# Optimization experiments

Hardware: AMD Instinct MI355X
Metric: run time of the kernel (lower is better)

Reference implementation:

```python
import jax, jax.numpy as jnp
import numpy as np

N, C, A, CI = 32768, 512, 64, 1024  # n_locations, content_size, address_size, controller_input_size
EPS = 1e-7


def setup_inputs() -> dict:
    key = jax.random.key(0)
    ks = jax.random.split(key, 12)
    g = lambda i, shape, s=1.0: jax.random.normal(ks[i], shape, dtype=jnp.float32) * s
    xav = lambda i, shape: g(i, shape, float(np.sqrt(2.0 / (shape[0] + shape[1]))))
    return {
        "controller_hidden_state": g(0, (N, 1)),
        "controller_input": g(1, (CI, 1)),
        "memory_contents": g(2, (N, C), 0.5),
        "memory_addresses": xav(3, (N, A)),
        "exp_mov_avg_similarity": g(4, (N, 1), 0.1),
        "W_query": xav(5, (C + A, N)),
        "b_query": jnp.zeros((C + A, 1), jnp.float32),
        "u_sharpen": xav(6, (1, N)),
        "b_sharpen": jnp.zeros((1,), jnp.float32),
        "u_lru": xav(7, (1, N)),
        "b_lru": jnp.zeros((1,), jnp.float32),
        "W_erase": xav(8, (C, N)),
        "b_erase": jnp.zeros((C, 1), jnp.float32),
        "W_content_hidden": xav(9, (C, N)),
        "W_content_input": xav(10, (C, CI)),
        "u_content_alpha": xav(11, (N + CI, 1)),
        "b_content_alpha": jnp.zeros((1, 1), jnp.float32),
    }


def reference(controller_hidden_state, controller_input, memory_contents, memory_addresses,
              exp_mov_avg_similarity, W_query, b_query, u_sharpen, b_sharpen, u_lru, b_lru,
              W_erase, b_erase, W_content_hidden, W_content_input, u_content_alpha,
              b_content_alpha):
    h, x = controller_hidden_state, controller_input
    # ---- address_memory ----
    full_mem = jnp.concatenate([memory_addresses, memory_contents], axis=1)  # [N, A+C]
    query = W_query @ h + b_query                                            # [A+C, 1]
    beta = jax.nn.softplus(u_sharpen @ h + b_sharpen) + 1.0                  # [1, 1]
    q = query[:, 0]
    q_norm = jnp.maximum(jnp.linalg.norm(q), EPS)
    m_norm = jnp.maximum(jnp.linalg.norm(full_mem, axis=1), EPS)             # [N]
    cos = (full_mem @ q) / (m_norm * q_norm)                                 # [N] cosine sim per location
    sim = (beta[0, 0] * cos)[:, None]                                        # [N, 1]
    gamma = jax.nn.sigmoid(u_lru @ h + b_lru)                                # [1, 1] LRU gate
    addr = jax.nn.softmax(sim - gamma * exp_mov_avg_similarity, axis=0)      # [N, 1]
    # (state buffer update, next-step only): new_ema = 0.1*ema + 0.9*sim
    # ---- update (vectorized erase/write over all N locations) ----
    erase = W_erase @ h + b_erase                                            # [C, 1]
    alpha = u_content_alpha.T @ jnp.concatenate([h, x], axis=0) + b_content_alpha  # [1, 1]
    cand = jax.nn.relu(W_content_hidden @ h + alpha * (W_content_input @ x))       # [C, 1]
    new_mem = (1.0 - addr * erase.T) * memory_contents + addr * cand.T       # [N, C]
    # ---- read (on updated memory) ----
    new_full = jnp.concatenate([memory_addresses, new_mem], axis=1)          # [N, A+C]
    read = new_full.T @ addr                                                 # [A+C, 1]
    return read
```

## Files before the change

### kernel.cpp

```cpp
#include <hip/hip_runtime.h>
#include <hip/hip_bf16.h>
#include <math.h>

#define NN 32768
#define CC 512
#define AA 64
#define CIN 1024
#define EPSV 1e-7f


#define QOFF 2128
#define STOFF 2704
#define SCOFF 4240
#define PAOFF 5264
#define PMOFF 38032

typedef float floatx4 __attribute__((ext_vector_type(4)));

__device__ __forceinline__ float4 ntload4(const float4* p) {
    floatx4 v = __builtin_nontemporal_load(reinterpret_cast<const floatx4*>(p));
    return make_float4(v.x, v.y, v.z, v.w);
}
__device__ __forceinline__ float ntloadf(const float* p) {
    return __builtin_nontemporal_load(p);
}

__global__ __launch_bounds__(256) void k1_gemv(
    const float* __restrict__ h, const float* __restrict__ x,
    const float* __restrict__ Wq, const float* __restrict__ Wer,
    const float* __restrict__ Wch, const float* __restrict__ Wci,
    const float* __restrict__ ush, const float* __restrict__ ulr,
    const float* __restrict__ uca, float* __restrict__ ws)
{
    const int b = blockIdx.x, tid = threadIdx.x;
    const int wave = tid >> 6, lane = tid & 63;
    __shared__ float hs[4096];
    __shared__ float red[4][8];

    if (b < 1600) {
        const int rg = b >> 3, chunk = b & 7;
        const float4* h4 = reinterpret_cast<const float4*>(h) + chunk * 1024;
        float4* hs4 = reinterpret_cast<float4*>(hs);
        #pragma unroll
        for (int k = 0; k < 4; ++k) hs4[k * 256 + tid] = h4[k * 256 + tid];
        __syncthreads();
        const int r0 = rg * 8;
        const float* mat; int base;
        if (r0 < 576)       { mat = Wq;  base = 0; }
        else if (r0 < 1088) { mat = Wer; base = 576; }
        else                { mat = Wch; base = 1088; }
        const float4* m4 = reinterpret_cast<const float4*>(
            mat + (size_t)(r0 - base) * NN + chunk * 4096);
        const int rs = NN / 4;
        float acc[8] = {0,0,0,0,0,0,0,0};
        float4 cur[8];
        #pragma unroll
        for (int r = 0; r < 8; ++r) cur[r] = ntload4(m4 + (size_t)r * rs + tid);
        #pragma unroll
        for (int it = 0; it < 4; ++it) {
            float4 nxt[8];
            if (it < 3) {
                #pragma unroll
                for (int r = 0; r < 8; ++r)
                    nxt[r] = ntload4(m4 + (size_t)r * rs + (it + 1) * 256 + tid);
            }
            float4 hb = hs4[it * 256 + tid];
            #pragma unroll
            for (int r = 0; r < 8; ++r)
                acc[r] += cur[r].x * hb.x + cur[r].y * hb.y +
                          cur[r].z * hb.z + cur[r].w * hb.w;
            if (it < 3) {
                #pragma unroll
                for (int r = 0; r < 8; ++r) cur[r] = nxt[r];
            }
        }
        #pragma unroll
        for (int r = 0; r < 8; ++r) {
            #pragma unroll
            for (int off = 32; off >= 1; off >>= 1)
                acc[r] += __shfl_xor(acc[r], off);
        }
        if (lane == 0) {
            #pragma unroll
            for (int r = 0; r < 8; ++r) red[wave][r] = acc[r];
        }
        __syncthreads();
        if (tid < 8) {
            float v = red[0][tid] + red[1][tid] + red[2][tid] + red[3][tid];
            atomicAdd(ws + r0 + tid, v);
        }
    } else if (b < 1664) {
        const int rg = b - 1600;
        float4 xv = reinterpret_cast<const float4*>(x)[tid];
        const float4* m4 = reinterpret_cast<const float4*>(
            Wci + (size_t)rg * 8 * CIN);
        float acc[8];
        #pragma unroll
        for (int r = 0; r < 8; ++r) {
            float4 a = ntload4(m4 + r * 256 + tid);
            acc[r] = a.x * xv.x + a.y * xv.y + a.z * xv.z + a.w * xv.w;
        }
        #pragma unroll
        for (int r = 0; r < 8; ++r) {
            #pragma unroll
            for (int off = 32; off >= 1; off >>= 1)
                acc[r] += __shfl_xor(acc[r], off);
        }
        if (lane == 0) {
            #pragma unroll
            for (int r = 0; r < 8; ++r) red[wave][r] = acc[r];
        }
        __syncthreads();
        if (tid < 8) {
            float v = red[0][tid] + red[1][tid] + red[2][tid] + red[3][tid];
            ws[1600 + rg * 8 + tid] = v;
        }
    } else {
        const int t = b - 1664, sd = t >> 3, chunk = t & 7;
        const float* vec = (sd == 0) ? ush : (sd == 1) ? ulr : uca;
        const float4* v4 = reinterpret_cast<const float4*>(vec) + chunk * 1024;
        const float4* h4 = reinterpret_cast<const float4*>(h) + chunk * 1024;
        float acc = 0.f;
        #pragma unroll
        for (int it = 0; it < 4; ++it) {
            float4 a = v4[it * 256 + tid];
            float4 hb = h4[it * 256 + tid];
            acc += a.x * hb.x + a.y * hb.y + a.z * hb.z + a.w * hb.w;
        }
        if (sd == 2 && chunk == 0) {
            float4 a = reinterpret_cast<const float4*>(uca)[NN / 4 + tid];
            float4 xv = reinterpret_cast<const float4*>(x)[tid];
            acc += a.x * xv.x + a.y * xv.y + a.z * xv.z + a.w * xv.w;
        }
        #pragma unroll
        for (int off = 32; off >= 1; off >>= 1)
            acc += __shfl_xor(acc, off);
        if (lane == 0) red[wave][0] = acc;
        __syncthreads();
        if (tid == 0)
            atomicAdd(ws + 2112 + sd,
                      red[0][0] + red[1][0] + red[2][0] + red[3][0]);
    }
}

__global__ __launch_bounds__(256) void k1b_scalars(
    const float* __restrict__ bq, const float* __restrict__ bsh,
    const float* __restrict__ blr, const float* __restrict__ bca,
    float* __restrict__ ws)
{
    __shared__ float red[256];
    const int tid = threadIdx.x;
    float s = 0.f;
    for (int j = tid; j < 576; j += 256) {
        float q = ws[j] + bq[j];
        ws[QOFF + j] = q;
        s += q * q;
    }
    red[tid] = s; __syncthreads();
    for (int st = 128; st > 0; st >>= 1) {
        if (tid < st) red[tid] += red[tid + st];
        __syncthreads();
    }
    if (tid == 0) {
        float qn = fmaxf(sqrtf(red[0]), EPSV);
        float bp = ws[2112] + bsh[0];
        float beta = (bp > 20.f ? bp : log1pf(expf(bp))) + 1.0f;
        float gp = ws[2113] + blr[0];
        float gamma = 1.f / (1.f + expf(-gp));
        float alpha = ws[2114] + bca[0];
        ws[2112] = beta; ws[2113] = gamma; ws[2114] = alpha; ws[2115] = qn;
    }
}

__global__ __launch_bounds__(512) void k2f_fused(
    const float* __restrict__ Mm, const float* __restrict__ Ad,
    const float* __restrict__ ema, const float* __restrict__ ws,
    float* __restrict__ pm, float* __restrict__ pa, float* __restrict__ stats)
{
    __shared__ float lw[8][1092];
    const int b = blockIdx.x, tid = threadIdx.x, wave = tid >> 6, lane = tid & 63;
    const float beta = ws[2112], gamma = ws[2113], qn = ws[2115];
    const float ql = ws[QOFF + lane];
    float4 qa = *reinterpret_cast<const float4*>(ws + QOFF + 64 + lane * 8);
    float4 qb = *reinterpret_cast<const float4*>(ws + QOFF + 68 + lane * 8);
    float qm[8] = {qa.x, qa.y, qa.z, qa.w, qb.x, qb.y, qb.z, qb.w};

    float a1[8] = {0,0,0,0,0,0,0,0};
    float a2[8] = {0,0,0,0,0,0,0,0};
    float aA = 0.f, m_run = -1e30f, Z = 0.f, S2 = 0.f;
    const int base = b * 64 + wave * 8;
    for (int j = 0; j < 8; ++j) {
        const int i = base + j;
        float a = ntloadf(Ad + (size_t)i * AA + lane);
        float4 m0 = ntload4(reinterpret_cast<const float4*>(Mm + (size_t)i * CC + lane * 8));
        float4 m1 = ntload4(reinterpret_cast<const float4*>(Mm + (size_t)i * CC + lane * 8 + 4));
        float mm[8] = {m0.x, m0.y, m0.z, m0.w, m1.x, m1.y, m1.z, m1.w};
        float dot = a * ql, nn = a * a;
        #pragma unroll
        for (int k = 0; k < 8; ++k) { float f = mm[k]; dot += f * qm[k]; nn += f * f; }
        #pragma unroll
        for (int off = 32; off >= 1; off >>= 1) {
            dot += __shfl_xor(dot, off);
            nn  += __shfl_xor(nn, off);
        }
        float mn = fmaxf(sqrtf(nn), EPSV);
        float s = beta * (dot / (mn * qn)) - gamma * ema[i];
        if (s > m_run) {
            float f = expf(m_run - s);
            float f2 = f * f;
            Z *= f; S2 *= f2; aA *= f;
            #pragma unroll
            for (int k = 0; k < 8; ++k) { a1[k] *= f; a2[k] *= f2; }
            m_run = s;
        }
        float w = expf(s - m_run);
        float w2 = w * w;
        Z += w; S2 += w2; aA += w * a;
        #pragma unroll
        for (int k = 0; k < 8; ++k) { a1[k] += w * mm[k]; a2[k] += w2 * mm[k]; }
    }
    #pragma unroll
    for (int k = 0; k < 8; ++k) {
        lw[wave][lane * 8 + k] = a1[k];
        lw[wave][512 + lane * 8 + k] = a2[k];
    }
    lw[wave][1024 + lane] = aA;
    if (lane == 0) { lw[wave][1088] = m_run; lw[wave][1089] = Z; lw[wave][1090] = S2; }
    __syncthreads();
    float mb = lw[0][1088];
    #pragma unroll
    for (int w = 1; w < 8; ++w) mb = fmaxf(mb, lw[w][1088]);
    float fw[8];
    #pragma unroll
    for (int w = 0; w < 8; ++w) fw[w] = expf(lw[w][1088] - mb);
    for (int e = tid; e < 1024; e += 512) {
        float v = 0.f;
        if (e < 512) {
            #pragma unroll
            for (int w = 0; w < 8; ++w) v += fw[w] * lw[w][e];
        } else {
            #pragma unroll
            for (int w = 0; w < 8; ++w) v += fw[w] * fw[w] * lw[w][e];
        }
        pm[(size_t)e * 512 + b] = v;
    }
    if (tid < 64) {
        float v = 0.f;
        #pragma unroll
        for (int w = 0; w < 8; ++w) v += fw[w] * lw[w][1024 + tid];
        pa[tid * 512 + b] = v;
    }
    if (tid == 0) {
        float Zl = 0.f, S2l = 0.f;
        #pragma unroll
        for (int w = 0; w < 8; ++w) {
            Zl  += fw[w] * lw[w][1089];
            S2l += fw[w] * fw[w] * lw[w][1090];
        }
        stats[b] = mb; stats[512 + b] = Zl; stats[1024 + b] = S2l;
    }
}

__global__ __launch_bounds__(512) void k3g(
    const float* __restrict__ stats, float* __restrict__ sc,
    float* __restrict__ ws)
{
    __shared__ float red[512];
    const int t = threadIdx.x;
    float m = stats[t];
    red[t] = m; __syncthreads();
    for (int st = 256; st > 0; st >>= 1) {
        if (t < st) red[t] = fmaxf(red[t], red[t + st]);
        __syncthreads();
    }
    float mx = red[0]; __syncthreads();
    float e1 = expf(m - mx);
    red[t] = e1 * stats[512 + t]; __syncthreads();
    for (int st = 256; st > 0; st >>= 1) {
        if (t < st) red[t] += red[t + st];
        __syncthreads();
    }
    float Zg = red[0]; __syncthreads();
    red[t] = e1 * e1 * stats[1024 + t]; __syncthreads();
    for (int st = 256; st > 0; st >>= 1) {
        if (t < st) red[t] += red[t + st];
        __syncthreads();
    }
    float S2s = red[0];
    float iZ = 1.f / Zg;
    sc[t] = e1 * iZ;
    sc[512 + t] = e1 * e1 * iZ * iZ;
    if (t == 0) ws[2118] = S2s * iZ * iZ;
}

__global__ __launch_bounds__(256) void k5_final(
    const float* __restrict__ ws, const float* __restrict__ pm,
    const float* __restrict__ pa, const float* __restrict__ sc,
    const float* __restrict__ ber, float* __restrict__ out)
{
    __shared__ float red[256];
    const int b = blockIdx.x, tid = threadIdx.x;
    if (b < 64) {
        float v = sc[tid] * pa[b * 512 + tid] + sc[tid + 256] * pa[b * 512 + tid + 256];
        red[tid] = v; __syncthreads();
        for (int st = 128; st > 0; st >>= 1) {
            if (tid < st) red[tid] += red[tid + st];
            __syncthreads();
        }
        if (tid == 0) out[b] = red[0];
    } else {
        const int c = b - 64;
        float v1 = sc[tid] * pm[(size_t)c * 512 + tid]
                 + sc[tid + 256] * pm[(size_t)c * 512 + tid + 256];
        float v2 = sc[512 + tid] * pm[(size_t)(512 + c) * 512 + tid]
                 + sc[512 + tid + 256] * pm[(size_t)(512 + c) * 512 + tid + 256];
        red[tid] = v1; __syncthreads();
        for (int st = 128; st > 0; st >>= 1) {
            if (tid < st) red[tid] += red[tid + st];
            __syncthreads();
        }
        float s1 = red[0];
        __syncthreads();
        red[tid] = v2; __syncthreads();
        for (int st = 128; st > 0; st >>= 1) {
            if (tid < st) red[tid] += red[tid + st];
            __syncthreads();
        }
        if (tid == 0) {
            float s2v = red[0];
            float er = ws[576 + c] + ber[c];
            float ch = ws[1088 + c], cx = ws[1600 + c];
            float alpha = ws[2114], S2 = ws[2118];
            float cand = fmaxf(ch + alpha * cx, 0.f);
            out[64 + c] = s1 - er * s2v + S2 * cand;
        }
    }
}

extern "C" void kernel_launch(void* const* d_in, const int* in_sizes, int n_in,
                              void* d_out, int out_size, void* d_ws, size_t ws_size,
                              hipStream_t stream)
{
    const float* h   = (const float*)d_in[0];
    const float* x   = (const float*)d_in[1];
    const float* Mm  = (const float*)d_in[2];
    const float* Ad  = (const float*)d_in[3];
    const float* ema = (const float*)d_in[4];
    const float* Wq  = (const float*)d_in[5];
    const float* bq  = (const float*)d_in[6];
    const float* ush = (const float*)d_in[7];
    const float* bsh = (const float*)d_in[8];
    const float* ulr = (const float*)d_in[9];
    const float* blr = (const float*)d_in[10];
    const float* Wer = (const float*)d_in[11];
    const float* ber = (const float*)d_in[12];
    const float* Wch = (const float*)d_in[13];
    const float* Wci = (const float*)d_in[14];
    const float* uca = (const float*)d_in[15];
    const float* bca = (const float*)d_in[16];

    float* ws    = (float*)d_ws;
    float* stats = ws + STOFF;
    float* sc    = ws + SCOFF;
    float* pa    = ws + PAOFF;
    float* pm    = ws + PMOFF;
    float* out   = (float*)d_out;

    (void)hipMemsetAsync(ws, 0, QOFF * sizeof(float), stream);

    hipLaunchKernelGGL(k1_gemv,     dim3(1688), dim3(256), 0, stream,
                       h, x, Wq, Wer, Wch, Wci, ush, ulr, uca, ws);
    hipLaunchKernelGGL(k1b_scalars, dim3(1),    dim3(256), 0, stream,
                       bq, bsh, blr, bca, ws);
    hipLaunchKernelGGL(k2f_fused,   dim3(512),  dim3(512), 0, stream,
                       Mm, Ad, ema, ws, pm, pa, stats);
    hipLaunchKernelGGL(k3g,         dim3(1),    dim3(512), 0, stream, stats, sc, ws);
    hipLaunchKernelGGL(k5_final,    dim3(576),  dim3(256), 0, stream,
                       ws, pm, pa, sc, ber, out);
}
```

Measured before the change: 281.3 us.

## Drop memset and two single-block kernels by writing per-chunk partials

The GEMV stage now writes per-chunk partial sums to distinct workspace slots instead of using atomicAdd. This removes the hipMemsetAsync that zeroed the accumulators. The scalar-prep kernel is folded into the prologue of the fused memory kernel, and the softmax-statistics kernel is recomputed redundantly in every block of the final kernel, leaving three launches instead of five plus a memset. Block reductions switch from shared-memory trees to wave shuffles. The cost is redundant per-block work: every block re-reduces the query partials, and 576 blocks each re-reduce the 512 softmax stats.

```diff
diff --git a/kernel.cpp b/kernel.cpp
--- a/kernel.cpp
+++ b/kernel.cpp
@@ -1,5 +1,4 @@
 #include <hip/hip_runtime.h>
-#include <hip/hip_bf16.h>
 #include <math.h>
 
 #define NN 32768
@@ -9,11 +8,12 @@
 #define EPSV 1e-7f
 
 
-#define QOFF 2128
-#define STOFF 2704
-#define SCOFF 4240
-#define PAOFF 5264
-#define PMOFF 38032
+#define DOTP  0
+#define SDOT  12800
+#define CONTX 12824
+#define STOFF 13344
+#define PAOFF 14912
+#define PMOFF 47680
 
 typedef float floatx4 __attribute__((ext_vector_type(4)));
 
@@ -87,7 +87,7 @@
         __syncthreads();
         if (tid < 8) {
             float v = red[0][tid] + red[1][tid] + red[2][tid] + red[3][tid];
-            atomicAdd(ws + r0 + tid, v);
+            ws[DOTP + chunk * 1600 + r0 + tid] = v;
         }
     } else if (b < 1664) {
         const int rg = b - 1600;
@@ -113,7 +113,7 @@
         __syncthreads();
         if (tid < 8) {
             float v = red[0][tid] + red[1][tid] + red[2][tid] + red[3][tid];
-            ws[1600 + rg * 8 + tid] = v;
+            ws[CONTX + rg * 8 + tid] = v;
         }
     } else {
         const int t = b - 1664, sd = t >> 3, chunk = t & 7;
@@ -138,51 +138,51 @@
         if (lane == 0) red[wave][0] = acc;
         __syncthreads();
         if (tid == 0)
-            atomicAdd(ws + 2112 + sd,
-                      red[0][0] + red[1][0] + red[2][0] + red[3][0]);
-    }
-}
-
-__global__ __launch_bounds__(256) void k1b_scalars(
-    const float* __restrict__ bq, const float* __restrict__ bsh,
-    const float* __restrict__ blr, const float* __restrict__ bca,
-    float* __restrict__ ws)
-{
-    __shared__ float red[256];
-    const int tid = threadIdx.x;
-    float s = 0.f;
-    for (int j = tid; j < 576; j += 256) {
-        float q = ws[j] + bq[j];
-        ws[QOFF + j] = q;
-        s += q * q;
-    }
-    red[tid] = s; __syncthreads();
-    for (int st = 128; st > 0; st >>= 1) {
-        if (tid < st) red[tid] += red[tid + st];
-        __syncthreads();
-    }
-    if (tid == 0) {
-        float qn = fmaxf(sqrtf(red[0]), EPSV);
-        float bp = ws[2112] + bsh[0];
-        float beta = (bp > 20.f ? bp : log1pf(expf(bp))) + 1.0f;
-        float gp = ws[2113] + blr[0];
-        float gamma = 1.f / (1.f + expf(-gp));
-        float alpha = ws[2114] + bca[0];
-        ws[2112] = beta; ws[2113] = gamma; ws[2114] = alpha; ws[2115] = qn;
+            ws[SDOT + sd * 8 + chunk] =
+                red[0][0] + red[1][0] + red[2][0] + red[3][0];
     }
 }
 
 __global__ __launch_bounds__(512) void k2f_fused(
     const float* __restrict__ Mm, const float* __restrict__ Ad,
     const float* __restrict__ ema, const float* __restrict__ ws,
+    const float* __restrict__ bq, const float* __restrict__ bsh,
+    const float* __restrict__ blr,
     float* __restrict__ pm, float* __restrict__ pa, float* __restrict__ stats)
 {
     __shared__ float lw[8][1092];
+    __shared__ __align__(16) float qsh[576];
+    __shared__ float r2[12];
     const int b = blockIdx.x, tid = threadIdx.x, wave = tid >> 6, lane = tid & 63;
-    const float beta = ws[2112], gamma = ws[2113], qn = ws[2115];
-    const float ql = ws[QOFF + lane];
-    float4 qa = *reinterpret_cast<const float4*>(ws + QOFF + 64 + lane * 8);
-    float4 qb = *reinterpret_cast<const float4*>(ws + QOFF + 68 + lane * 8);
+
+    float qq = 0.f;
+    for (int j = tid; j < 576; j += 512) {
+        float s = bq[j];
+        #pragma unroll
+        for (int c = 0; c < 8; ++c) s += ws[DOTP + c * 1600 + j];
+        qsh[j] = s;
+        qq += s * s;
+    }
+    #pragma unroll
+    for (int off = 32; off >= 1; off >>= 1) qq += __shfl_xor(qq, off);
+    if (lane == 0) r2[wave] = qq;
+    __syncthreads();
+    if (tid == 0) {
+        float qn2 = 0.f;
+        #pragma unroll
+        for (int w = 0; w < 8; ++w) qn2 += r2[w];
+        float bp = bsh[0], gp = blr[0];
+        #pragma unroll
+        for (int c = 0; c < 8; ++c) { bp += ws[SDOT + c]; gp += ws[SDOT + 8 + c]; }
+        r2[8]  = fmaxf(sqrtf(qn2), EPSV);
+        r2[9]  = (bp > 20.f ? bp : log1pf(expf(bp))) + 1.0f;
+        r2[10] = 1.f / (1.f + expf(-gp));
+    }
+    __syncthreads();
+    const float qn = r2[8], beta = r2[9], gamma = r2[10];
+    const float ql = qsh[lane];
+    float4 qa = *reinterpret_cast<const float4*>(qsh + 64 + lane * 8);
+    float4 qb = *reinterpret_cast<const float4*>(qsh + 68 + lane * 8);
     float qm[8] = {qa.x, qa.y, qa.z, qa.w, qb.x, qb.y, qb.z, qb.w};
 
     float a1[8] = {0,0,0,0,0,0,0,0};
@@ -261,76 +261,69 @@
     }
 }
 
-__global__ __launch_bounds__(512) void k3g(
-    const float* __restrict__ stats, float* __restrict__ sc,
-    float* __restrict__ ws)
-{
-    __shared__ float red[512];
-    const int t = threadIdx.x;
-    float m = stats[t];
-    red[t] = m; __syncthreads();
-    for (int st = 256; st > 0; st >>= 1) {
-        if (t < st) red[t] = fmaxf(red[t], red[t + st]);
-        __syncthreads();
-    }
-    float mx = red[0]; __syncthreads();
-    float e1 = expf(m - mx);
-    red[t] = e1 * stats[512 + t]; __syncthreads();
-    for (int st = 256; st > 0; st >>= 1) {
-        if (t < st) red[t] += red[t + st];
-        __syncthreads();
-    }
-    float Zg = red[0]; __syncthreads();
-    red[t] = e1 * e1 * stats[1024 + t]; __syncthreads();
-    for (int st = 256; st > 0; st >>= 1) {
-        if (t < st) red[t] += red[t + st];
-        __syncthreads();
-    }
-    float S2s = red[0];
-    float iZ = 1.f / Zg;
-    sc[t] = e1 * iZ;
-    sc[512 + t] = e1 * e1 * iZ * iZ;
-    if (t == 0) ws[2118] = S2s * iZ * iZ;
-}
-
 __global__ __launch_bounds__(256) void k5_final(
     const float* __restrict__ ws, const float* __restrict__ pm,
-    const float* __restrict__ pa, const float* __restrict__ sc,
-    const float* __restrict__ ber, float* __restrict__ out)
+    const float* __restrict__ pa, const float* __restrict__ ber,
+    const float* __restrict__ bca, float* __restrict__ out)
 {
-    __shared__ float red[256];
-    const int b = blockIdx.x, tid = threadIdx.x;
+    __shared__ float red[20];
+    const int b = blockIdx.x, tid = threadIdx.x, wave = tid >> 6, lane = tid & 63;
+    const float* stats = ws + STOFF;
+
+    float m1 = stats[tid], m2 = stats[256 + tid];
+    float mv = fmaxf(m1, m2);
+    #pragma unroll
+    for (int off = 32; off >= 1; off >>= 1) mv = fmaxf(mv, __shfl_xor(mv, off));
+    if (lane == 0) red[wave] = mv;
+    __syncthreads();
+    const float mx = fmaxf(fmaxf(red[0], red[1]), fmaxf(red[2], red[3]));
+    float e1 = expf(m1 - mx), e2 = expf(m2 - mx);
+    float zs = e1 * stats[512 + tid]  + e2 * stats[768 + tid];
+    float ss = e1 * e1 * stats[1024 + tid] + e2 * e2 * stats[1280 + tid];
+    #pragma unroll
+    for (int off = 32; off >= 1; off >>= 1) {
+        zs += __shfl_xor(zs, off);
+        ss += __shfl_xor(ss, off);
+    }
+    if (lane == 0) { red[4 + wave] = zs; red[8 + wave] = ss; }
+    __syncthreads();
+    const float Zg  = red[4] + red[5] + red[6] + red[7];
+    const float S2s = red[8] + red[9] + red[10] + red[11];
+    const float iZ = 1.f / Zg;
+    const float sct = e1 * iZ, sct2 = e2 * iZ;
+
     if (b < 64) {
-        float v = sc[tid] * pa[b * 512 + tid] + sc[tid + 256] * pa[b * 512 + tid + 256];
-        red[tid] = v; __syncthreads();
-        for (int st = 128; st > 0; st >>= 1) {
-            if (tid < st) red[tid] += red[tid + st];
-            __syncthreads();
-        }
-        if (tid == 0) out[b] = red[0];
+        float v = sct * pa[b * 512 + tid] + sct2 * pa[b * 512 + 256 + tid];
+        #pragma unroll
+        for (int off = 32; off >= 1; off >>= 1) v += __shfl_xor(v, off);
+        if (lane == 0) red[12 + wave] = v;
+        __syncthreads();
+        if (tid == 0) out[b] = red[12] + red[13] + red[14] + red[15];
     } else {
         const int c = b - 64;
-        float v1 = sc[tid] * pm[(size_t)c * 512 + tid]
-                 + sc[tid + 256] * pm[(size_t)c * 512 + tid + 256];
-        float v2 = sc[512 + tid] * pm[(size_t)(512 + c) * 512 + tid]
-                 + sc[512 + tid + 256] * pm[(size_t)(512 + c) * 512 + tid + 256];
-        red[tid] = v1; __syncthreads();
-        for (int st = 128; st > 0; st >>= 1) {
-            if (tid < st) red[tid] += red[tid + st];
-            __syncthreads();
-        }
-        float s1 = red[0];
-        __syncthreads();
-        red[tid] = v2; __syncthreads();
-        for (int st = 128; st > 0; st >>= 1) {
-            if (tid < st) red[tid] += red[tid + st];
-            __syncthreads();
-        }
+        float v1 = sct * pm[(size_t)c * 512 + tid]
+                 + sct2 * pm[(size_t)c * 512 + 256 + tid];
+        float v2 = sct * sct * pm[(size_t)(512 + c) * 512 + tid]
+                 + sct2 * sct2 * pm[(size_t)(512 + c) * 512 + 256 + tid];
+        #pragma unroll
+        for (int off = 32; off >= 1; off >>= 1) {
+            v1 += __shfl_xor(v1, off);
+            v2 += __shfl_xor(v2, off);
+        }
+        if (lane == 0) { red[12 + wave] = v1; red[16 + wave] = v2; }
+        __syncthreads();
         if (tid == 0) {
-            float s2v = red[0];
-            float er = ws[576 + c] + ber[c];
-            float ch = ws[1088 + c], cx = ws[1600 + c];
-            float alpha = ws[2114], S2 = ws[2118];
+            float s1  = red[12] + red[13] + red[14] + red[15];
+            float s2v = red[16] + red[17] + red[18] + red[19];
+            float er = ber[c], ch = 0.f, alpha = bca[0];
+            #pragma unroll
+            for (int p = 0; p < 8; ++p) {
+                er    += ws[DOTP + p * 1600 + 576 + c];
+                ch    += ws[DOTP + p * 1600 + 1088 + c];
+                alpha += ws[SDOT + 16 + p];
+            }
+            float cx = ws[CONTX + c];
+            float S2 = S2s * iZ * iZ;
             float cand = fmaxf(ch + alpha * cx, 0.f);
             out[64 + c] = s1 - er * s2v + S2 * cand;
         }
@@ -361,20 +354,14 @@
 
     float* ws    = (float*)d_ws;
     float* stats = ws + STOFF;
-    float* sc    = ws + SCOFF;
     float* pa    = ws + PAOFF;
     float* pm    = ws + PMOFF;
     float* out   = (float*)d_out;
 
-    (void)hipMemsetAsync(ws, 0, QOFF * sizeof(float), stream);
-
-    hipLaunchKernelGGL(k1_gemv,     dim3(1688), dim3(256), 0, stream,
+    hipLaunchKernelGGL(k1_gemv,   dim3(1688), dim3(256), 0, stream,
                        h, x, Wq, Wer, Wch, Wci, ush, ulr, uca, ws);
-    hipLaunchKernelGGL(k1b_scalars, dim3(1),    dim3(256), 0, stream,
-                       bq, bsh, blr, bca, ws);
-    hipLaunchKernelGGL(k2f_fused,   dim3(512),  dim3(512), 0, stream,
-                       Mm, Ad, ema, ws, pm, pa, stats);
-    hipLaunchKernelGGL(k3g,         dim3(1),    dim3(512), 0, stream, stats, sc, ws);
-    hipLaunchKernelGGL(k5_final,    dim3(576),  dim3(256), 0, stream,
-                       ws, pm, pa, sc, ber, out);
-}
+    hipLaunchKernelGGL(k2f_fused, dim3(512),  dim3(512), 0, stream,
+                       Mm, Ad, ema, ws, bq, bsh, blr, pm, pa, stats);
+    hipLaunchKernelGGL(k5_final,  dim3(576),  dim3(256), 0, stream,
+                       ws, pm, pa, ber, bca, out);
+}
```

Result: faster. 274.4 us (-2.5%).
